# Kernel optimization log

Hardware: AMD Instinct MI355X
Metric: run time of the kernel (lower is better)

Reference implementation:

```python
import jax, jax.numpy as jnp
import numpy as np

N_NODES = 50000


def gcn_conv(x, edge_index, W, b):
    """PyG GCNConv: add self-loops, symmetric deg^-1/2 normalization,
    linear transform, scatter-add aggregation."""
    n = x.shape[0]
    src, dst = edge_index[0], edge_index[1]
    loop = jnp.arange(n, dtype=src.dtype)
    src = jnp.concatenate([src, loop])          # [E+N]
    dst = jnp.concatenate([dst, loop])          # [E+N]
    w = jnp.ones(src.shape[0], dtype=x.dtype)   # edge_weight=None -> ones
    deg = jax.ops.segment_sum(w, dst, num_segments=n)          # [N]
    dinv = jnp.where(deg > 0, jax.lax.rsqrt(deg), 0.0)
    norm = dinv[src] * w * dinv[dst]            # [E+N]
    h = x @ W                                   # [N, out]
    msg = h[src] * norm[:, None]                # [E+N, out] gather + scale
    out = jax.ops.segment_sum(msg, dst, num_segments=n)        # scatter-add
    return out + b


def setup_inputs() -> dict:
    key = jax.random.key(0)
    k1, k2, k3, k4, k5, k6 = jax.random.split(key, 6)
    in_c, hid_c, out_c = 3, 128, 64
    n_edges = 800000
    x = jax.random.normal(k1, (N_NODES, in_c), dtype=jnp.float32)
    edge_index = jax.random.randint(k2, (2, n_edges), 0, N_NODES, dtype=jnp.int64)
    W1 = jax.random.normal(k3, (in_c, hid_c), dtype=jnp.float32) / np.sqrt(in_c)
    b1 = jnp.zeros((hid_c,), dtype=jnp.float32)
    W2 = jax.random.normal(k4, (hid_c, out_c), dtype=jnp.float32) / np.sqrt(hid_c)
    b2 = jnp.zeros((out_c,), dtype=jnp.float32)
    return {"x": x, "edge_index": edge_index, "W1": W1, "b1": b1, "W2": W2, "b2": b2}


def reference(x, edge_index, W1, b1, W2, b2):
    h = gcn_conv(x, edge_index, W1, b1)
    h = jax.nn.relu(h)
    return gcn_conv(h, edge_index, W2, b2)
```

## Files before the change

kernel.cpp:

```cpp
#include <hip/hip_runtime.h>
#include <hip/hip_bf16.h>

#define HID 128
#define OUTC 64
#define INC 3
#define BCAP 64
#define OVF_CAP 8192
#define NT 64
#define NCBMAX 256
#define CAP8K 8192
#define KPT 8
#define EPT 4

static __device__ __forceinline__ unsigned short f2bf(float f) {
    __hip_bfloat16 b = __float2bfloat16(f);
    return *reinterpret_cast<unsigned short*>(&b);
}
static __device__ __forceinline__ float bf2f(unsigned short u) {
    __hip_bfloat16 b = *reinterpret_cast<__hip_bfloat16*>(&u);
    return __bfloat162float(b);
}


__global__ __launch_bounds__(256) void place2_kernel(const int* __restrict__ src,
                                                     const int* __restrict__ dst, int E, int NCB,
                                                     int* __restrict__ cbcur,
                                                     unsigned int* __restrict__ part,
                                                     int* __restrict__ ovf, int* __restrict__ ovf_cnt) {
    __shared__ int lhist[NCBMAX];
    __shared__ int lbase[NCBMAX];
    int t = threadIdx.x;
    int s0 = blockIdx.x * (256 * KPT);
    for (int i = t; i < NCBMAX; i += 256) lhist[i] = 0;
    __syncthreads();

    unsigned pk[KPT];
    int cbv[KPT];
    bool val[KPT];
#pragma unroll
    for (int i = 0; i < KPT; ++i) {
        int e = s0 + t + i * 256;
        val[i] = (e < E);
        if (val[i]) {
            int d = dst[e], s = src[e];
            cbv[i] = d >> 8;
            pk[i] = (unsigned)s | ((unsigned)(d & 255) << 16);
            atomicAdd(&lhist[cbv[i]], 1);
        }
    }
    __syncthreads();
    for (int i = t; i < NCB; i += 256) {
        int c = lhist[i];
        lbase[i] = c ? atomicAdd(&cbcur[i], c) : 0;
        lhist[i] = 0;
    }
    __syncthreads();
#pragma unroll
    for (int i = 0; i < KPT; ++i) {
        if (val[i]) {
            int cb = cbv[i];
            int p = atomicAdd(&lhist[cb], 1);
            int slot = lbase[cb] + p;
            if (slot < CAP8K) {
                part[(size_t)cb * CAP8K + slot] = pk[i];
            } else {
                int o = atomicAdd(ovf_cnt, 1);
                if (o < OVF_CAP) {
                    ovf[2 * o] = (int)(pk[i] & 0xFFFF);
                    ovf[2 * o + 1] = cb * 256 + (int)((pk[i] >> 16) & 0xFF);
                }
            }
        }
    }
}

__global__ __launch_bounds__(256) void bin_kernel(const unsigned int* __restrict__ part,
                                                  const int* __restrict__ cbcur,
                                                  const float* __restrict__ x, int N,
                                                  int* __restrict__ cursor,
                                                  unsigned short* __restrict__ bucket,
                                                  float4* __restrict__ z4,
                                                  int* __restrict__ ovf, int* __restrict__ ovf_cnt) {
    __shared__ int lcnt[256];
    __shared__ unsigned short lbuck[256 * BCAP];
    int cb = blockIdx.x, t = threadIdx.x;
    lcnt[t] = 0;
    __syncthreads();
    int cnt = cbcur[cb];
    cnt = cnt < CAP8K ? cnt : CAP8K;
    size_t start = (size_t)cb * CAP8K;
    for (int i = t; i < cnt; i += 256) {
        unsigned pk = part[start + i];
        int s = pk & 0xFFFF;
        int ln = (pk >> 16) & 0xFF;
        int p = atomicAdd(&lcnt[ln], 1);
        if (p < BCAP) {
            lbuck[ln * BCAP + p] = (unsigned short)s;
        } else {
            int o = atomicAdd(ovf_cnt, 1);
            if (o < OVF_CAP) { ovf[2 * o] = s; ovf[2 * o + 1] = cb * 256 + ln; }
        }
    }
    __syncthreads();
    int d = cb * 256 + t;
    if (d < N) {
        int deg = lcnt[t];
        cursor[d] = deg;
        float dd = rsqrtf((float)(deg + 1));
        z4[d] = make_float4(dd * x[3 * d], dd * x[3 * d + 1], dd * x[3 * d + 2], dd);
    }
    const uint4* lsrc = (const uint4*)lbuck;
    uint4* gdst = (uint4*)(bucket + (size_t)cb * 256 * BCAP);
    for (int i = t; i < (256 * BCAP * 2) / 16; i += 256) gdst[i] = lsrc[i];
}


template <typename IT>
__global__ void fill_bucket_kernel(const int* __restrict__ src, const int* __restrict__ dst, int E,
                                   int T, int* __restrict__ cursor, IT* __restrict__ bucket,
                                   int* __restrict__ ovf, int* __restrict__ ovf_cnt) {
    int tid = blockIdx.x * blockDim.x + threadIdx.x;
    int d[EPT], s[EPT], p[EPT];
    bool v[EPT];
#pragma unroll
    for (int k = 0; k < EPT; ++k) {
        int e = tid + k * T;
        v[k] = (e < E);
        d[k] = v[k] ? dst[e] : 0;
        s[k] = v[k] ? src[e] : 0;
    }
#pragma unroll
    for (int k = 0; k < EPT; ++k)
        if (v[k]) p[k] = atomicAdd(&cursor[d[k]], 1);
#pragma unroll
    for (int k = 0; k < EPT; ++k) {
        if (v[k]) {
            if (p[k] < BCAP) {
                bucket[(size_t)d[k] * BCAP + p[k]] = (IT)s[k];
            } else {
                int o = atomicAdd(ovf_cnt, 1);
                if (o < OVF_CAP) { ovf[2 * o] = s[k]; ovf[2 * o + 1] = d[k]; }
            }
        }
    }
}

__global__ void z4_kernel(const float* __restrict__ x, const int* __restrict__ cursor,
                          float4* __restrict__ z4, int N) {
    int i = blockIdx.x * blockDim.x + threadIdx.x;
    if (i < N) {
        float dd = rsqrtf((float)(cursor[i] + 1));
        z4[i] = make_float4(dd * x[3 * i], dd * x[3 * i + 1], dd * x[3 * i + 2], dd);
    }
}


template <typename IT>
__global__ __launch_bounds__(256) void hidden_kernel(const IT* __restrict__ bucket,
                                                     const int* __restrict__ cursor,
                                                     const float4* __restrict__ z4,
                                                     const float* __restrict__ W1,
                                                     const float* __restrict__ b1,
                                                     const float* __restrict__ W2,
                                                     unsigned short* __restrict__ hs2b, int N,
                                                     const int* __restrict__ ovf,
                                                     const int* __restrict__ ovf_cnt) {
    __shared__ float h_s[HID][NT];
    __shared__ float w_s[HID * OUTC];
    float* u_s = &h_s[0][0];
    int t = threadIdx.x;
    int base = blockIdx.x * NT;

    for (int i = t; i < HID * OUTC; i += 256) w_s[i] = W2[i];

    {
        int g = (t & 63) & 15;
        int r = (t & 63) >> 4;
        int n = (t >> 6) * 16 + g;
        int d = base + n;
        float p0 = 0.f, p1 = 0.f, p2 = 0.f;
        if (d < N) {
            int cnt = cursor[d];
            cnt = cnt < BCAP ? cnt : BCAP;
            for (int k = r; k < cnt; k += 4) {
                int s = (int)bucket[(size_t)d * BCAP + k];
                float4 zv = z4[s];
                p0 += zv.x; p1 += zv.y; p2 += zv.z;
            }
        }
        p0 += __shfl_xor(p0, 16, 64); p0 += __shfl_xor(p0, 32, 64);
        p1 += __shfl_xor(p1, 16, 64); p1 += __shfl_xor(p1, 32, 64);
        p2 += __shfl_xor(p2, 16, 64); p2 += __shfl_xor(p2, 32, 64);
        if (r == 0 && d < N) {
            int oc = *ovf_cnt;
            if (oc > 0) {
                oc = oc < OVF_CAP ? oc : OVF_CAP;
                for (int i = 0; i < oc; ++i) {
                    if (ovf[2 * i + 1] == d) {
                        float4 zs = z4[ovf[2 * i]];
                        p0 += zs.x; p1 += zs.y; p2 += zs.z;
                    }
                }
            }
            u_s[n * 3 + 0] = p0;
            u_s[n * 3 + 1] = p1;
            u_s[n * 3 + 2] = p2;
        }
    }
    __syncthreads();

    int n = t & 63;
    int d = base + n;
    float u0 = 0.f, u1 = 0.f, u2 = 0.f;
    if (d < N) {
        float a0 = u_s[n * 3], a1 = u_s[n * 3 + 1], a2 = u_s[n * 3 + 2];
        float4 zv = z4[d];
        float dd = zv.w;
        u0 = dd * (a0 + zv.x);
        u1 = dd * (a1 + zv.y);
        u2 = dd * (a2 + zv.z);
    }
    __syncthreads();

    {
        int k0 = t >> 6;
#pragma unroll
        for (int i = 0; i < HID / 4; ++i) {
            int k = k0 + 4 * i;
            float v = u0 * W1[k] + u1 * W1[HID + k] + u2 * W1[2 * HID + k] + b1[k];
            h_s[k][n] = fmaxf(v, 0.f);
        }
    }
    __syncthreads();

    int tx = t & 15, ty = t >> 4;
    float acc[4][4] = {};
#pragma unroll 8
    for (int k = 0; k < HID; ++k) {
        float4 hv = *(const float4*)&h_s[k][ty * 4];
        float4 wv = *(const float4*)&w_s[k * OUTC + tx * 4];
        float hr[4] = {hv.x, hv.y, hv.z, hv.w};
        float wr[4] = {wv.x, wv.y, wv.z, wv.w};
#pragma unroll
        for (int r = 0; r < 4; ++r)
#pragma unroll
            for (int c = 0; c < 4; ++c) acc[r][c] = fmaf(hr[r], wr[c], acc[r][c]);
    }

#pragma unroll
    for (int r = 0; r < 4; ++r) {
        int nn = ty * 4 + r;
        int dd_i = base + nn;
        if (dd_i < N) {
            float dd = z4[dd_i].w;
            ushort4 o;
            o.x = f2bf(dd * acc[r][0]);
            o.y = f2bf(dd * acc[r][1]);
            o.z = f2bf(dd * acc[r][2]);
            o.w = f2bf(dd * acc[r][3]);
            *(ushort4*)&hs2b[(size_t)dd_i * OUTC + tx * 4] = o;
        }
    }
}


#define ACC8(u)                                                        \
    do {                                                               \
        a0 += bf2f((u).x & 0xFFFF); a1 += bf2f((u).x >> 16);           \
        a2 += bf2f((u).y & 0xFFFF); a3 += bf2f((u).y >> 16);           \
        a4 += bf2f((u).z & 0xFFFF); a5 += bf2f((u).z >> 16);           \
        a6 += bf2f((u).w & 0xFFFF); a7 += bf2f((u).w >> 16);           \
    } while (0)

template <typename IT>
__global__ __launch_bounds__(256) void gather2_kernel(const int* __restrict__ cursor,
                                                      const IT* __restrict__ bucket,
                                                      const uint4* __restrict__ hs2q,
                                                      const float4* __restrict__ z4,
                                                      const float* __restrict__ b2,
                                                      float* __restrict__ out, int N,
                                                      const int* __restrict__ ovf,
                                                      const int* __restrict__ ovf_cnt) {
    __shared__ int slist[32 * BCAP];
    int t = threadIdx.x;
    int base = blockIdx.x * 32;
    int lim = (N - base) * BCAP;
    int total = 32 * BCAP;
    if (lim > total) lim = total;
    for (int i = t; i < lim; i += 256) slist[i] = (int)bucket[(size_t)base * BCAP + i];
    __syncthreads();

    int g = t >> 3;
    int q = t & 7;
    int d = base + g;
    if (d >= N) return;
    int cnt = cursor[d];
    cnt = cnt < BCAP ? cnt : BCAP;
    const int* my = &slist[g * BCAP];
    float a0 = 0.f, a1 = 0.f, a2 = 0.f, a3 = 0.f, a4 = 0.f, a5 = 0.f, a6 = 0.f, a7 = 0.f;
    int k = 0;
    for (; k + 8 <= cnt; k += 8) {
        uint4 u0 = hs2q[(size_t)my[k]     * 8 + q];
        uint4 u1 = hs2q[(size_t)my[k + 1] * 8 + q];
        uint4 u2 = hs2q[(size_t)my[k + 2] * 8 + q];
        uint4 u3 = hs2q[(size_t)my[k + 3] * 8 + q];
        uint4 u4 = hs2q[(size_t)my[k + 4] * 8 + q];
        uint4 u5 = hs2q[(size_t)my[k + 5] * 8 + q];
        uint4 u6 = hs2q[(size_t)my[k + 6] * 8 + q];
        uint4 u7 = hs2q[(size_t)my[k + 7] * 8 + q];
        ACC8(u0); ACC8(u1); ACC8(u2); ACC8(u3);
        ACC8(u4); ACC8(u5); ACC8(u6); ACC8(u7);
    }
    for (; k + 4 <= cnt; k += 4) {
        uint4 u0 = hs2q[(size_t)my[k]     * 8 + q];
        uint4 u1 = hs2q[(size_t)my[k + 1] * 8 + q];
        uint4 u2 = hs2q[(size_t)my[k + 2] * 8 + q];
        uint4 u3 = hs2q[(size_t)my[k + 3] * 8 + q];
        ACC8(u0); ACC8(u1); ACC8(u2); ACC8(u3);
    }
    for (; k < cnt; ++k) {
        uint4 u = hs2q[(size_t)my[k] * 8 + q];
        ACC8(u);
    }
    int oc = *ovf_cnt;
    if (oc > 0) {
        oc = oc < OVF_CAP ? oc : OVF_CAP;
        for (int i = 0; i < oc; ++i) {
            if (ovf[2 * i + 1] == d) {
                uint4 u = hs2q[(size_t)ovf[2 * i] * 8 + q];
                ACC8(u);
            }
        }
    }
    uint4 us = hs2q[(size_t)d * 8 + q];
    float dd = z4[d].w;
    float4 bbl = *(const float4*)&b2[8 * q];
    float4 bbh = *(const float4*)&b2[8 * q + 4];
    float4 ol, oh;
    ol.x = dd * (a0 + bf2f(us.x & 0xFFFF)) + bbl.x;
    ol.y = dd * (a1 + bf2f(us.x >> 16)) + bbl.y;
    ol.z = dd * (a2 + bf2f(us.y & 0xFFFF)) + bbl.z;
    ol.w = dd * (a3 + bf2f(us.y >> 16)) + bbl.w;
    oh.x = dd * (a4 + bf2f(us.z & 0xFFFF)) + bbh.x;
    oh.y = dd * (a5 + bf2f(us.z >> 16)) + bbh.y;
    oh.z = dd * (a6 + bf2f(us.w & 0xFFFF)) + bbh.z;
    oh.w = dd * (a7 + bf2f(us.w >> 16)) + bbh.w;
    *(float4*)&out[(size_t)d * OUTC + 8 * q] = ol;
    *(float4*)&out[(size_t)d * OUTC + 8 * q + 4] = oh;
}

static inline size_t align256(size_t v) { return (v + 255) & ~(size_t)255; }

extern "C" void kernel_launch(void* const* d_in, const int* in_sizes, int n_in,
                              void* d_out, int out_size, void* d_ws, size_t ws_size,
                              hipStream_t stream) {
    const float* x  = (const float*)d_in[0];
    const int*   ei = (const int*)d_in[1];
    const float* W1 = (const float*)d_in[2];
    const float* b1 = (const float*)d_in[3];
    const float* W2 = (const float*)d_in[4];
    const float* b2 = (const float*)d_in[5];
    float* out = (float*)d_out;

    const int N = in_sizes[0] / INC;
    const int E = in_sizes[1] / 2;
    const int* src = ei;
    const int* dst = ei + E;
    const bool u16 = (N <= 65535);
    const int NCB = (N + 255) >> 8;

    char* ws = (char*)d_ws;
    size_t off = 0;
    int*    cursor  = (int*)(ws + off);    off += align256((size_t)N * 4);
    float4* z4      = (float4*)(ws + off); off += align256((size_t)N * 16);
    int*    cbcur   = (int*)(ws + off);    off += (size_t)NCBMAX * 4;
    int*    ovf_cnt = (int*)(ws + off);    off += 256;
    int*    ovf     = (int*)(ws + off);    off += (size_t)OVF_CAP * 8;
    unsigned int* part = (unsigned int*)(ws + off);
    off += align256(u16 ? (size_t)NCB * CAP8K * 4 : 0);
    void*   bucket  = (void*)(ws + off);
    off += align256(u16 ? (size_t)NCB * 256 * BCAP * 2 : (size_t)N * BCAP * 4);
    unsigned short* hs2b = (unsigned short*)(ws + off); off += (size_t)N * OUTC * 2;
    const uint4* hs2q = (const uint4*)hs2b;

    const int B = 256;

    if (u16) {
        hipMemsetAsync(cbcur, 0, (size_t)NCBMAX * 4 + 256, stream);
        int NB = (E + 256 * KPT - 1) / (256 * KPT);
        place2_kernel<<<NB, B, 0, stream>>>(src, dst, E, NCB, cbcur, part, ovf, ovf_cnt);
        bin_kernel<<<NCB, B, 0, stream>>>(part, cbcur, x, N, cursor,
                                          (unsigned short*)bucket, z4, ovf, ovf_cnt);
    } else {
        hipMemsetAsync(cursor, 0, (size_t)N * sizeof(int), stream);
        hipMemsetAsync(ovf_cnt, 0, 64, stream);
        int grid = (E + B * EPT - 1) / (B * EPT);
        int T = grid * B;
        fill_bucket_kernel<int><<<grid, B, 0, stream>>>(src, dst, E, T, cursor, (int*)bucket,
                                                        ovf, ovf_cnt);
        z4_kernel<<<(N + B - 1) / B, B, 0, stream>>>(x, cursor, z4, N);
    }

    if (u16)
        hidden_kernel<unsigned short><<<(N + NT - 1) / NT, 256, 0, stream>>>(
            (const unsigned short*)bucket, cursor, z4, W1, b1, W2, hs2b, N, ovf, ovf_cnt);
    else
        hidden_kernel<int><<<(N + NT - 1) / NT, 256, 0, stream>>>(
            (const int*)bucket, cursor, z4, W1, b1, W2, hs2b, N, ovf, ovf_cnt);

    if (u16)
        gather2_kernel<unsigned short><<<(N + 31) / 32, B, 0, stream>>>(
            cursor, (const unsigned short*)bucket, hs2q, z4, b2, out, N, ovf, ovf_cnt);
    else
        gather2_kernel<int><<<(N + 31) / 32, B, 0, stream>>>(
            cursor, (const int*)bucket, hs2q, z4, b2, out, N, ovf, ovf_cnt);
}
```

Measured before the change: 137.8 us.

## Split layer-2 feature table into two half-width tables gathered in separate passes

The hidden kernel now writes the bf16 layer-2 features into two separate arrays, each holding 32 channels per node, and the gather kernel runs twice, once per half, writing its own 32 output columns. Each pass gathers from a 3.2MB table instead of a 6.4MB one, which is meant to improve cache hit rates for the random neighbor reads. In exchange it launches one more kernel and reads the bucket lists, cursor and overflow data twice, and each random access is now an 8-byte load instead of a 16-byte one.

```diff
diff --git a/kernel.cpp b/kernel.cpp
--- a/kernel.cpp
+++ b/kernel.cpp
@@ -162,7 +162,8 @@
                                                      const float* __restrict__ W1,
                                                      const float* __restrict__ b1,
                                                      const float* __restrict__ W2,
-                                                     unsigned short* __restrict__ hs2b, int N,
+                                                     unsigned short* __restrict__ hsA,
+                                                     unsigned short* __restrict__ hsB, int N,
                                                      const int* __restrict__ ovf,
                                                      const int* __restrict__ ovf_cnt) {
     __shared__ float h_s[HID][NT];
@@ -247,6 +248,8 @@
             for (int c = 0; c < 4; ++c) acc[r][c] = fmaf(hr[r], wr[c], acc[r][c]);
     }
 
+    unsigned short* tb = (tx < 8) ? hsA : hsB;
+    int txl = tx & 7;
 #pragma unroll
     for (int r = 0; r < 4; ++r) {
         int nn = ty * 4 + r;
@@ -258,27 +261,25 @@
             o.y = f2bf(dd * acc[r][1]);
             o.z = f2bf(dd * acc[r][2]);
             o.w = f2bf(dd * acc[r][3]);
-            *(ushort4*)&hs2b[(size_t)dd_i * OUTC + tx * 4] = o;
-        }
-    }
-}
-
-
-#define ACC8(u)                                                        \
+            *(ushort4*)&tb[(size_t)dd_i * 32 + txl * 4] = o;
+        }
+    }
+}
+
+
+#define ACC4(u)                                                        \
     do {                                                               \
         a0 += bf2f((u).x & 0xFFFF); a1 += bf2f((u).x >> 16);           \
         a2 += bf2f((u).y & 0xFFFF); a3 += bf2f((u).y >> 16);           \
-        a4 += bf2f((u).z & 0xFFFF); a5 += bf2f((u).z >> 16);           \
-        a6 += bf2f((u).w & 0xFFFF); a7 += bf2f((u).w >> 16);           \
     } while (0)
 
 template <typename IT>
 __global__ __launch_bounds__(256) void gather2_kernel(const int* __restrict__ cursor,
                                                       const IT* __restrict__ bucket,
-                                                      const uint4* __restrict__ hs2q,
+                                                      const uint2* __restrict__ hsv,
                                                       const float4* __restrict__ z4,
                                                       const float* __restrict__ b2,
-                                                      float* __restrict__ out, int N,
+                                                      float* __restrict__ out, int N, int foff,
                                                       const int* __restrict__ ovf,
                                                       const int* __restrict__ ovf_cnt) {
     __shared__ int slist[32 * BCAP];
@@ -297,56 +298,50 @@
     int cnt = cursor[d];
     cnt = cnt < BCAP ? cnt : BCAP;
     const int* my = &slist[g * BCAP];
-    float a0 = 0.f, a1 = 0.f, a2 = 0.f, a3 = 0.f, a4 = 0.f, a5 = 0.f, a6 = 0.f, a7 = 0.f;
+    float a0 = 0.f, a1 = 0.f, a2 = 0.f, a3 = 0.f;
     int k = 0;
     for (; k + 8 <= cnt; k += 8) {
-        uint4 u0 = hs2q[(size_t)my[k]     * 8 + q];
-        uint4 u1 = hs2q[(size_t)my[k + 1] * 8 + q];
-        uint4 u2 = hs2q[(size_t)my[k + 2] * 8 + q];
-        uint4 u3 = hs2q[(size_t)my[k + 3] * 8 + q];
-        uint4 u4 = hs2q[(size_t)my[k + 4] * 8 + q];
-        uint4 u5 = hs2q[(size_t)my[k + 5] * 8 + q];
-        uint4 u6 = hs2q[(size_t)my[k + 6] * 8 + q];
-        uint4 u7 = hs2q[(size_t)my[k + 7] * 8 + q];
-        ACC8(u0); ACC8(u1); ACC8(u2); ACC8(u3);
-        ACC8(u4); ACC8(u5); ACC8(u6); ACC8(u7);
+        uint2 u0 = hsv[(size_t)my[k]     * 8 + q];
+        uint2 u1 = hsv[(size_t)my[k + 1] * 8 + q];
+        uint2 u2 = hsv[(size_t)my[k + 2] * 8 + q];
+        uint2 u3 = hsv[(size_t)my[k + 3] * 8 + q];
+        uint2 u4 = hsv[(size_t)my[k + 4] * 8 + q];
+        uint2 u5 = hsv[(size_t)my[k + 5] * 8 + q];
+        uint2 u6 = hsv[(size_t)my[k + 6] * 8 + q];
+        uint2 u7 = hsv[(size_t)my[k + 7] * 8 + q];
+        ACC4(u0); ACC4(u1); ACC4(u2); ACC4(u3);
+        ACC4(u4); ACC4(u5); ACC4(u6); ACC4(u7);
     }
     for (; k + 4 <= cnt; k += 4) {
-        uint4 u0 = hs2q[(size_t)my[k]     * 8 + q];
-        uint4 u1 = hs2q[(size_t)my[k + 1] * 8 + q];
-        uint4 u2 = hs2q[(size_t)my[k + 2] * 8 + q];
-        uint4 u3 = hs2q[(size_t)my[k + 3] * 8 + q];
-        ACC8(u0); ACC8(u1); ACC8(u2); ACC8(u3);
+        uint2 u0 = hsv[(size_t)my[k]     * 8 + q];
+        uint2 u1 = hsv[(size_t)my[k + 1] * 8 + q];
+        uint2 u2 = hsv[(size_t)my[k + 2] * 8 + q];
+        uint2 u3 = hsv[(size_t)my[k + 3] * 8 + q];
+        ACC4(u0); ACC4(u1); ACC4(u2); ACC4(u3);
     }
     for (; k < cnt; ++k) {
-        uint4 u = hs2q[(size_t)my[k] * 8 + q];
-        ACC8(u);
+        uint2 u = hsv[(size_t)my[k] * 8 + q];
+        ACC4(u);
     }
     int oc = *ovf_cnt;
     if (oc > 0) {
         oc = oc < OVF_CAP ? oc : OVF_CAP;
         for (int i = 0; i < oc; ++i) {
             if (ovf[2 * i + 1] == d) {
-                uint4 u = hs2q[(size_t)ovf[2 * i] * 8 + q];
-                ACC8(u);
+                uint2 u = hsv[(size_t)ovf[2 * i] * 8 + q];
+                ACC4(u);
             }
         }
     }
-    uint4 us = hs2q[(size_t)d * 8 + q];
+    uint2 us = hsv[(size_t)d * 8 + q];
     float dd = z4[d].w;
-    float4 bbl = *(const float4*)&b2[8 * q];
-    float4 bbh = *(const float4*)&b2[8 * q + 4];
-    float4 ol, oh;
-    ol.x = dd * (a0 + bf2f(us.x & 0xFFFF)) + bbl.x;
-    ol.y = dd * (a1 + bf2f(us.x >> 16)) + bbl.y;
-    ol.z = dd * (a2 + bf2f(us.y & 0xFFFF)) + bbl.z;
-    ol.w = dd * (a3 + bf2f(us.y >> 16)) + bbl.w;
-    oh.x = dd * (a4 + bf2f(us.z & 0xFFFF)) + bbh.x;
-    oh.y = dd * (a5 + bf2f(us.z >> 16)) + bbh.y;
-    oh.z = dd * (a6 + bf2f(us.w & 0xFFFF)) + bbh.z;
-    oh.w = dd * (a7 + bf2f(us.w >> 16)) + bbh.w;
-    *(float4*)&out[(size_t)d * OUTC + 8 * q] = ol;
-    *(float4*)&out[(size_t)d * OUTC + 8 * q + 4] = oh;
+    float4 bb = *(const float4*)&b2[foff + 4 * q];
+    float4 o;
+    o.x = dd * (a0 + bf2f(us.x & 0xFFFF)) + bb.x;
+    o.y = dd * (a1 + bf2f(us.x >> 16)) + bb.y;
+    o.z = dd * (a2 + bf2f(us.y & 0xFFFF)) + bb.z;
+    o.w = dd * (a3 + bf2f(us.y >> 16)) + bb.w;
+    *(float4*)&out[(size_t)d * OUTC + foff + 4 * q] = o;
 }
 
 static inline size_t align256(size_t v) { return (v + 255) & ~(size_t)255; }
@@ -380,8 +375,8 @@
     off += align256(u16 ? (size_t)NCB * CAP8K * 4 : 0);
     void*   bucket  = (void*)(ws + off);
     off += align256(u16 ? (size_t)NCB * 256 * BCAP * 2 : (size_t)N * BCAP * 4);
-    unsigned short* hs2b = (unsigned short*)(ws + off); off += (size_t)N * OUTC * 2;
-    const uint4* hs2q = (const uint4*)hs2b;
+    unsigned short* hsA = (unsigned short*)(ws + off); off += align256((size_t)N * 32 * 2);
+    unsigned short* hsB = (unsigned short*)(ws + off); off += align256((size_t)N * 32 * 2);
 
     const int B = 256;
 
@@ -403,15 +398,23 @@
 
     if (u16)
         hidden_kernel<unsigned short><<<(N + NT - 1) / NT, 256, 0, stream>>>(
-            (const unsigned short*)bucket, cursor, z4, W1, b1, W2, hs2b, N, ovf, ovf_cnt);
+            (const unsigned short*)bucket, cursor, z4, W1, b1, W2, hsA, hsB, N, ovf, ovf_cnt);
     else
         hidden_kernel<int><<<(N + NT - 1) / NT, 256, 0, stream>>>(
-            (const int*)bucket, cursor, z4, W1, b1, W2, hs2b, N, ovf, ovf_cnt);
-
-    if (u16)
-        gather2_kernel<unsigned short><<<(N + 31) / 32, B, 0, stream>>>(
-            cursor, (const unsigned short*)bucket, hs2q, z4, b2, out, N, ovf, ovf_cnt);
-    else
-        gather2_kernel<int><<<(N + 31) / 32, B, 0, stream>>>(
-            cursor, (const int*)bucket, hs2q, z4, b2, out, N, ovf, ovf_cnt);
-}
+            (const int*)bucket, cursor, z4, W1, b1, W2, hsA, hsB, N, ovf, ovf_cnt);
+
+    int g2grid = (N + 31) / 32;
+    if (u16) {
+        gather2_kernel<unsigned short><<<g2grid, B, 0, stream>>>(
+            cursor, (const unsigned short*)bucket, (const uint2*)hsA, z4, b2, out, N, 0,
+            ovf, ovf_cnt);
+        gather2_kernel<unsigned short><<<g2grid, B, 0, stream>>>(
+            cursor, (const unsigned short*)bucket, (const uint2*)hsB, z4, b2, out, N, 32,
+            ovf, ovf_cnt);
+    } else {
+        gather2_kernel<int><<<g2grid, B, 0, stream>>>(
+            cursor, (const int*)bucket, (const uint2*)hsA, z4, b2, out, N, 0, ovf, ovf_cnt);
+        gather2_kernel<int><<<g2grid, B, 0, stream>>>(
+            cursor, (const int*)bucket, (const uint2*)hsB, z4, b2, out, N, 32, ovf, ovf_cnt);
+    }
+}
```

Result: slower. 145.1 us (+5.3%).
